# Kernel optimization log

Hardware: AMD Instinct MI355X
Metric: run time of the kernel (lower is better)

The kernel has to match this reference:

```python
import jax, jax.numpy as jnp
import numpy as np

D = 512
H = 8
DH = D // H  # 64


def setup_inputs() -> dict:
    key = jax.random.key(0)
    ks = jax.random.split(key, 7)
    batch, la, lb = 8, 256, 256
    A = jax.random.normal(ks[0], (batch, la, D), dtype=jnp.float32)
    B = jax.random.normal(ks[1], (batch, lb, D), dtype=jnp.float32)
    s = 1.0 / np.sqrt(D)
    W1 = jax.random.uniform(ks[2], (D, D), minval=-s, maxval=s, dtype=jnp.float32)
    b1 = jax.random.uniform(ks[3], (D,), minval=-s, maxval=s, dtype=jnp.float32)
    W2 = jax.random.uniform(ks[4], (D, D), minval=-s, maxval=s, dtype=jnp.float32)
    b2 = jax.random.uniform(ks[5], (D,), minval=-s, maxval=s, dtype=jnp.float32)
    q = jax.random.normal(ks[6], (DH,), dtype=jnp.float32) * 0.1
    return {"A": A, "B": B, "W1": W1, "b1": b1, "W2": W2, "b2": b2, "q": q}


def reference(A, B, W1, b1, W2, b2, q):
    bs, la, _ = A.shape
    lb = B.shape[1]
    # Linear + ReLU, then raw row-major reshape to (batch, heads, len, dh)
    # (matches torch .view semantics: NOT a head-transpose split)
    A_ = jax.nn.relu(A @ W1.T + b1).reshape(bs, H, la, DH)
    B_ = jax.nn.relu(B @ W2.T + b2).reshape(bs, H, lb, DH)
    # bilinear score: tanh of elementwise pairwise product, dotted with q
    # att_maps: [bs, H, la, lb]
    att_maps = jnp.einsum(
        "bhijc,c->bhij",
        jnp.tanh(A_[:, :, :, None, :] * B_[:, :, None, :, :]),
        q,
    )
    temp_b2a = jax.nn.softmax(jnp.mean(att_maps, axis=3), axis=2)  # [bs,H,la]
    temp_a2b = jax.nn.softmax(jnp.mean(att_maps, axis=2), axis=2)  # [bs,H,lb]
    A_heads = A.reshape(bs, H, la, DH)
    B_heads = B.reshape(bs, H, lb, DH)
    A_p = jnp.sum(A_heads * temp_b2a[..., None], axis=2).reshape(bs, -1)  # [bs, d]
    B_p = jnp.sum(B_heads * temp_a2b[..., None], axis=2).reshape(bs, -1)  # [bs, d]
    return (
        jnp.concatenate((A_p, B_p), axis=1),
        jnp.mean(temp_b2a, axis=1),
        jnp.mean(temp_a2b, axis=1),
    )
```

## Files before the change

kernel.cpp:

```cpp
#include <hip/hip_runtime.h>
#include <hip/hip_bf16.h>

#define LOG2E 1.4426950408889634f
#define SC2   2.8853900817779268f

typedef __attribute__((ext_vector_type(8))) short short8b;
typedef __attribute__((ext_vector_type(4))) float f32x4;

__device__ __forceinline__ float fast_exp2(float x) {
#if __has_builtin(__builtin_amdgcn_exp2f)
  return __builtin_amdgcn_exp2f(x);
#else
  return exp2f(x);
#endif
}
__device__ __forceinline__ float fast_rcp(float x) {
#if __has_builtin(__builtin_amdgcn_rcpf)
  return __builtin_amdgcn_rcpf(x);
#else
  return 1.0f / x;
#endif
}
__device__ __forceinline__ short f2bf(float f) {
  __hip_bfloat16 h = __float2bfloat16(f);
  return *reinterpret_cast<short*>(&h);
}

__global__ __launch_bounds__(256) void cvt_kernel(
    const float* __restrict__ A, const float* __restrict__ B,
    const float* __restrict__ W1, const float* __restrict__ W2,
    short* __restrict__ Abf, short* __restrict__ Bbf,
    short* __restrict__ W1bf, short* __restrict__ W2bf) {
  int gid = blockIdx.x * 256 + threadIdx.x;
  const float* src; short* dst; int off;
  if (gid < 131072)      { src = A;  dst = Abf;  off = gid << 3; }
  else if (gid < 262144) { src = B;  dst = Bbf;  off = (gid - 131072) << 3; }
  else if (gid < 294912) { src = W1; dst = W1bf; off = (gid - 262144) << 3; }
  else                   { src = W2; dst = W2bf; off = (gid - 294912) << 3; }
  float4 v0 = *reinterpret_cast<const float4*>(src + off);
  float4 v1 = *reinterpret_cast<const float4*>(src + off + 4);
  short8b s = {f2bf(v0.x), f2bf(v0.y), f2bf(v0.z), f2bf(v0.w),
               f2bf(v1.x), f2bf(v1.y), f2bf(v1.z), f2bf(v1.w)};
  *reinterpret_cast<short8b*>(dst + off) = s;
}

__global__ __launch_bounds__(256) void gemm_fused_kernel(
    const short* __restrict__ Xa, const short* __restrict__ Wa,
    const float* __restrict__ ba, float* __restrict__ Oa,
    const short* __restrict__ Xb, const short* __restrict__ Wb,
    const float* __restrict__ bb, const float* __restrict__ q,
    float2* __restrict__ Cb, unsigned* __restrict__ Cnt,
    float* __restrict__ Ksum) {
  const int isB = blockIdx.z;
  const short* X = isB ? Xb : Xa;
  const short* W = isB ? Wb : Wa;
  const float* bias = isB ? bb : ba;

  __shared__ __align__(16) float Btile[64][65];
  __shared__ float qls[64];

  int t = threadIdx.x;
  int m0 = blockIdx.x * 64, n0 = blockIdx.y * 64;
  int l = t & 63, w = t >> 6;
  int wm = (w >> 1) * 32, wn = (w & 1) * 32;
  int lr = l & 15, ko = (l >> 4) * 8;

  if (isB && t < 64) qls[t] = q[t];

  f32x4 acc[2][2];
#pragma unroll
  for (int m = 0; m < 2; ++m)
#pragma unroll
    for (int n = 0; n < 2; ++n) acc[m][n] = f32x4{0.f, 0.f, 0.f, 0.f};

  const short* pA = X + (m0 + wm + lr) * 512 + ko;
  const short* pW = W + (n0 + wn + lr) * 512 + ko;

#pragma unroll
  for (int k0 = 0; k0 < 512; k0 += 32) {
    short8b a0 = *reinterpret_cast<const short8b*>(pA + k0);
    short8b a1 = *reinterpret_cast<const short8b*>(pA + 8192 + k0);
    short8b b0 = *reinterpret_cast<const short8b*>(pW + k0);
    short8b b1 = *reinterpret_cast<const short8b*>(pW + 8192 + k0);
    acc[0][0] = __builtin_amdgcn_mfma_f32_16x16x32_bf16(a0, b0, acc[0][0], 0, 0, 0);
    acc[0][1] = __builtin_amdgcn_mfma_f32_16x16x32_bf16(a0, b1, acc[0][1], 0, 0, 0);
    acc[1][0] = __builtin_amdgcn_mfma_f32_16x16x32_bf16(a1, b0, acc[1][0], 0, 0, 0);
    acc[1][1] = __builtin_amdgcn_mfma_f32_16x16x32_bf16(a1, b1, acc[1][1], 0, 0, 0);
  }

  if (!isB) {
#pragma unroll
    for (int n = 0; n < 2; ++n) {
      int col = n0 + wn + n * 16 + lr;
      float bv = bias[col];
#pragma unroll
      for (int m = 0; m < 2; ++m) {
        int rbase = m0 + wm + m * 16 + (l >> 4) * 4;
#pragma unroll
        for (int r = 0; r < 4; ++r) {
          float v = acc[m][n][r] + bv;
          Oa[(rbase + r) * 512 + col] = v > 0.f ? v : 0.f;
        }
      }
    }
    return;
  }

#pragma unroll
  for (int n = 0; n < 2; ++n) {
    int col = wn + n * 16 + lr;
    float bv = bias[n0 + col];
#pragma unroll
    for (int m = 0; m < 2; ++m) {
      int rbase = wm + m * 16 + (l >> 4) * 4;
#pragma unroll
      for (int r = 0; r < 4; ++r) {
        float v = acc[m][n][r] + bv;
        Btile[rbase + r][col] = v > 0.f ? v : 0.f;
      }
    }
  }
  __syncthreads();

  int jl = t >> 2, p = t & 2 ? (t & 3) : (t & 3);
  p = t & 3;
  int row = m0 + jl;
  int bh = (row >> 8) * 8 + ((row >> 5) & 7);
  int j = ((row & 31) << 3) + (n0 >> 6);
  int c0 = p * 16;

  int nz = 0;
  float K = 0.f;
#pragma unroll
  for (int cc = 0; cc < 16; ++cc) {
    float v = Btile[jl][c0 + cc];
    if (v > 0.f) { ++nz; K += qls[c0 + cc]; }
  }
  int incl = nz;
#pragma unroll
  for (int d = 1; d < 4; d <<= 1) {
    int u = __shfl_up(incl, d, 4);
    if (p >= d) incl += u;
  }
  int off = incl - nz;
  int total = __shfl(incl, 3, 4);

  float2* dst = Cb + (bh * 256 + j) * 64;
  int k = off;
#pragma unroll
  for (int cc = 0; cc < 16; ++cc) {
    int c = c0 + cc;
    float v = Btile[jl][c];
    if (v > 0.f) {
      unsigned qb = (__float_as_uint(-2.f * qls[c]) & ~63u) | (unsigned)c;
      dst[k] = make_float2(v * SC2, __uint_as_float(qb));
      ++k;
    }
  }
  K += __shfl_xor(K, 1, 4);
  K += __shfl_xor(K, 2, 4);
  if (p == 3) {
    int cnt = total;
    while (cnt & 3) { dst[cnt] = make_float2(0.f, 0.f); ++cnt; }
    Cnt[bh * 256 + j] = (unsigned)cnt;
    Ksum[bh * 256 + j] = K;
  }
}

__global__ __launch_bounds__(512, 8) void attmap_kernel(
    const float* __restrict__ Ar, const float2* __restrict__ Cb,
    const unsigned* __restrict__ Cnt,
    float* __restrict__ rowpart, float* __restrict__ colsum) {
  int bh = blockIdx.x, jblk = blockIdx.y, isplit = blockIdx.z;
  int t = threadIdx.x;
  int il = t & 127;
  int g = __builtin_amdgcn_readfirstlane(t >> 7);
  __shared__ __align__(16) float Als[128 * 65];
  __shared__ float red[512];
  __shared__ float cpart[8][8];

  const float* Abase = Ar + bh * 16384 + isplit * 8192;
#pragma unroll
  for (int it = 0; it < 4; ++it) {
    int idx = it * 512 + t;
    int r = idx >> 4, c4 = (idx & 15) << 2;
    float4 v = *reinterpret_cast<const float4*>(&Abase[r * 64 + c4]);
    Als[r * 65 + c4 + 0] = v.x; Als[r * 65 + c4 + 1] = v.y;
    Als[r * 65 + c4 + 2] = v.z; Als[r * 65 + c4 + 3] = v.w;
  }
  __syncthreads();

  const float* Arow = &Als[il * 65];
  float acc[8];

#pragma unroll
  for (int jj = 0; jj < 8; ++jj) {
    int jl = g * 8 + jj;
    int n = (int)__builtin_amdgcn_readfirstlane(Cnt[bh * 256 + jblk * 32 + jl]);
    const float4* P4 = reinterpret_cast<const float4*>(Cb + (bh * 256 + jblk * 32 + jl) * 64);
    float s0 = 0.f, s1 = 0.f;
    if (n > 0) {
      const int nit = n >> 2;
      float4 u0 = P4[0], v0 = P4[1];
      int i1 = (1 < nit) ? 1 : (nit - 1);
      float4 u1 = P4[i1 * 2], v1 = P4[i1 * 2 + 1];
#pragma unroll 1
      for (int it = 0; it < nit; ++it) {
        int i2 = it + 2; i2 = (i2 < nit) ? i2 : (nit - 1);
        float4 u2 = P4[i2 * 2], v2 = P4[i2 * 2 + 1];
        float g0 = Arow[__float_as_uint(u0.y) & 63u];
        float g1 = Arow[__float_as_uint(u0.w) & 63u];
        float g2 = Arow[__float_as_uint(v0.y) & 63u];
        float g3 = Arow[__float_as_uint(v0.w) & 63u];
        float e0 = fast_exp2(g0 * u0.x);
        float e1 = fast_exp2(g1 * u0.z);
        float e2 = fast_exp2(g2 * v0.x);
        float e3 = fast_exp2(g3 * v0.z);
        float w0 = e0 + 1.f, w1 = e1 + 1.f, w2 = e2 + 1.f, w3 = e3 + 1.f;
        float n01 = fmaf(u0.w, w0, u0.y * w1);
        float n23 = fmaf(v0.w, w2, v0.y * w3);
        s0 = fmaf(n01, fast_rcp(w0 * w1), s0);
        s1 = fmaf(n23, fast_rcp(w2 * w3), s1);
        u0 = u1; v0 = v1; u1 = u2; v1 = v2;
      }
    }
    acc[jj] = s0 + s1;
  }

  float rs = 0.f;
#pragma unroll
  for (int jj = 0; jj < 8; ++jj) rs += acc[jj];
  red[t] = rs;

  int lane = t & 63, w = t >> 6;
#pragma unroll
  for (int jj = 0; jj < 8; ++jj) {
    float v = acc[jj];
#pragma unroll
    for (int off = 32; off >= 1; off >>= 1) v += __shfl_xor(v, off);
    if (lane == 0) cpart[w][jj] = v;
  }
  __syncthreads();
  if (t < 128) {
    rowpart[(bh * 8 + jblk) * 256 + isplit * 128 + t] =
        red[t] + red[t + 128] + red[t + 256] + red[t + 384];
  } else if (t < 160) {
    int jl = t - 128;
    int gg = jl >> 3, jj = jl & 7;
    colsum[(bh * 2 + isplit) * 256 + jblk * 32 + jl] =
        cpart[2 * gg][jj] + cpart[2 * gg + 1][jj];
  }
}

__global__ __launch_bounds__(512) void softmax_pool_kernel(
    const float* __restrict__ rowpart, const float* __restrict__ colsum,
    const float* __restrict__ Ksum,
    const float* __restrict__ A0, const float* __restrict__ B0,
    float* __restrict__ b2a, float* __restrict__ a2b,
    float* __restrict__ poolA, float* __restrict__ poolB) {
  int bh = blockIdx.x, chunk = blockIdx.y;
  int b = bh >> 3, h = bh & 7;
  int t = threadIdx.x;
  int tt = t & 255;
  int lane = t & 63, w = (t >> 6) & 3;
  __shared__ float redA[4], redB[4], redC[4], redD[4];
  __shared__ float tA[256], tB[256];
  __shared__ float pp[8][64];

  float r = 0.f;
#pragma unroll
  for (int jb = 0; jb < 8; ++jb) r += rowpart[(bh * 8 + jb) * 256 + tt];
  r *= (1.f / 256.f);
  float cs = Ksum[bh * 256 + tt] +
             (colsum[(bh * 2 + 0) * 256 + tt] + colsum[(bh * 2 + 1) * 256 + tt]) * (1.f / 256.f);

  float mr = r, mc = cs;
#pragma unroll
  for (int off = 32; off >= 1; off >>= 1) {
    mr = fmaxf(mr, __shfl_xor(mr, off));
    mc = fmaxf(mc, __shfl_xor(mc, off));
  }
  if (lane == 0) { redA[w] = mr; redB[w] = mc; }
  __syncthreads();
  mr = fmaxf(fmaxf(redA[0], redA[1]), fmaxf(redA[2], redA[3]));
  mc = fmaxf(fmaxf(redB[0], redB[1]), fmaxf(redB[2], redB[3]));

  float er = fast_exp2((r - mr) * LOG2E);
  float ec = fast_exp2((cs - mc) * LOG2E);
  float sr = er, sc = ec;
#pragma unroll
  for (int off = 32; off >= 1; off >>= 1) {
    sr += __shfl_xor(sr, off);
    sc += __shfl_xor(sc, off);
  }
  if (lane == 0) { redC[w] = sr; redD[w] = sc; }
  __syncthreads();
  sr = redC[0] + redC[1] + redC[2] + redC[3];
  sc = redD[0] + redD[1] + redD[2] + redD[3];

  float vb2a = er * fast_rcp(sr);
  float va2b = ec * fast_rcp(sc);
  tA[tt] = vb2a; tB[tt] = va2b;
  if (chunk == 0) {
    b2a[bh * 256 + tt] = vb2a;
    a2b[bh * 256 + tt] = va2b;
  }
  __syncthreads();

  int c = t & 63, isub = t >> 6;
  const float* Ab = A0 + b * 131072 + h * 16384;
  const float* Bb = B0 + b * 131072 + h * 16384;
  float pa = 0.f, pb = 0.f;
#pragma unroll
  for (int ii = 0; ii < 8; ++ii) {
    int i = chunk * 64 + isub * 8 + ii;
    pa = fmaf(Ab[i * 64 + c], tA[i], pa);
    pb = fmaf(Bb[i * 64 + c], tB[i], pb);
  }
  pp[isub][c] = pa;
  __syncthreads();
  if (t < 64) {
    float s = 0.f;
#pragma unroll
    for (int k = 0; k < 8; ++k) s += pp[k][t];
    poolA[(bh * 4 + chunk) * 64 + t] = s;
  }
  __syncthreads();
  pp[isub][c] = pb;
  __syncthreads();
  if (t < 64) {
    float s = 0.f;
#pragma unroll
    for (int k = 0; k < 8; ++k) s += pp[k][t];
    poolB[(bh * 4 + chunk) * 64 + t] = s;
  }
}

__global__ __launch_bounds__(256) void final_kernel(
    const float* __restrict__ poolA, const float* __restrict__ poolB,
    const float* __restrict__ b2a, const float* __restrict__ a2b,
    float* __restrict__ out) {
  int b = blockIdx.x, t = threadIdx.x;
  float s1 = 0.f, s2 = 0.f;
#pragma unroll
  for (int h = 0; h < 8; ++h) {
    s1 += b2a[(b * 8 + h) * 256 + t];
    s2 += a2b[(b * 8 + h) * 256 + t];
  }
  out[8192 + b * 256 + t] = s1 * 0.125f;
  out[10240 + b * 256 + t] = s2 * 0.125f;

#pragma unroll
  for (int hh = 0; hh < 2; ++hh) {
    int idx = hh * 256 + t;
    int h = idx >> 6, c = idx & 63;
    int base = ((b * 8 + h) * 4) * 64 + c;
    float sA = poolA[base] + poolA[base + 64] + poolA[base + 128] + poolA[base + 192];
    float sB = poolB[base] + poolB[base + 64] + poolB[base + 128] + poolB[base + 192];
    out[b * 1024 + h * 64 + c] = sA;
    out[b * 1024 + 512 + h * 64 + c] = sB;
  }
}

extern "C" void kernel_launch(void* const* d_in, const int* in_sizes, int n_in,
                              void* d_out, int out_size, void* d_ws, size_t ws_size,
                              hipStream_t stream) {
  const float* A  = (const float*)d_in[0];
  const float* B  = (const float*)d_in[1];
  const float* W1 = (const float*)d_in[2];
  const float* b1 = (const float*)d_in[3];
  const float* W2 = (const float*)d_in[4];
  const float* b2 = (const float*)d_in[5];
  const float* q  = (const float*)d_in[6];
  float* out = (float*)d_out;
  float* ws = (float*)d_ws;

  float*    Ar      = ws;
  short*    Abf     = (short*)(ws + 1048576);
  short*    Bbf     = (short*)(ws + 1572864);
  short*    W1bf    = (short*)(ws + 2097152);
  short*    W2bf    = (short*)(ws + 2228224);
  float2*   Cb      = (float2*)(ws + 2359296);
  unsigned* Cnt     = (unsigned*)(ws + 4456448);
  float*    Ksum    = ws + 4472832;
  float*    rowpart = ws + 4489216;
  float*    colsum  = ws + 4620288;
  float*    b2a     = ws + 4653056;
  float*    a2b     = ws + 4669440;
  float*    poolA   = ws + 4685824;
  float*    poolB   = ws + 4702208;

  cvt_kernel<<<1280, 256, 0, stream>>>(A, B, W1, W2, Abf, Bbf, W1bf, W2bf);
  gemm_fused_kernel<<<dim3(32, 8, 2), 256, 0, stream>>>(
      Abf, W1bf, b1, Ar, Bbf, W2bf, b2, q, Cb, Cnt, Ksum);
  attmap_kernel<<<dim3(64, 8, 2), 512, 0, stream>>>(Ar, Cb, Cnt, rowpart, colsum);
  softmax_pool_kernel<<<dim3(64, 4), 512, 0, stream>>>(
      rowpart, colsum, Ksum, A, B, b2a, a2b, poolA, poolB);
  final_kernel<<<8, 256, 0, stream>>>(poolA, poolB, b2a, a2b, out);
}
```

Before: 74.33 us.

## Stage GEMM tiles through LDS and enlarge block tile to 128x64

The fused linear GEMM now loads each 32-wide K slice of X and W into shared memory cooperatively, then feeds MFMA fragments from LDS instead of loading them directly from global memory per wave. The block tile grows from 64 to 128 rows, so each wave computes a 64x32 sub-tile, and the grid is halved. The compaction epilogue is remapped to two threads per row. This raises operand reuse and cuts redundant global loads, but adds two barriers per K step with no double buffering, uses more LDS, and launches fewer blocks (256 in total).

Result: faster. 70.18 us (-5.6%).

```diff
diff --git a/kernel.cpp b/kernel.cpp
--- a/kernel.cpp
+++ b/kernel.cpp
@@ -56,36 +56,53 @@
   const short* W = isB ? Wb : Wa;
   const float* bias = isB ? bb : ba;
 
-  __shared__ __align__(16) float Btile[64][65];
+  __shared__ __align__(16) short As[128 * 40];
+  __shared__ __align__(16) short Ws[64 * 40];
+  __shared__ __align__(16) float Btile[128][65];
   __shared__ float qls[64];
 
   int t = threadIdx.x;
-  int m0 = blockIdx.x * 64, n0 = blockIdx.y * 64;
+  int m0 = blockIdx.x * 128, n0 = blockIdx.y * 64;
   int l = t & 63, w = t >> 6;
-  int wm = (w >> 1) * 32, wn = (w & 1) * 32;
+  int wm = (w >> 1) * 64, wn = (w & 1) * 32;
   int lr = l & 15, ko = (l >> 4) * 8;
 
   if (isB && t < 64) qls[t] = q[t];
 
-  f32x4 acc[2][2];
-#pragma unroll
-  for (int m = 0; m < 2; ++m)
+  f32x4 acc[4][2];
+#pragma unroll
+  for (int m = 0; m < 4; ++m)
 #pragma unroll
     for (int n = 0; n < 2; ++n) acc[m][n] = f32x4{0.f, 0.f, 0.f, 0.f};
 
-  const short* pA = X + (m0 + wm + lr) * 512 + ko;
-  const short* pW = W + (n0 + wn + lr) * 512 + ko;
-
-#pragma unroll
   for (int k0 = 0; k0 < 512; k0 += 32) {
-    short8b a0 = *reinterpret_cast<const short8b*>(pA + k0);
-    short8b a1 = *reinterpret_cast<const short8b*>(pA + 8192 + k0);
-    short8b b0 = *reinterpret_cast<const short8b*>(pW + k0);
-    short8b b1 = *reinterpret_cast<const short8b*>(pW + 8192 + k0);
-    acc[0][0] = __builtin_amdgcn_mfma_f32_16x16x32_bf16(a0, b0, acc[0][0], 0, 0, 0);
-    acc[0][1] = __builtin_amdgcn_mfma_f32_16x16x32_bf16(a0, b1, acc[0][1], 0, 0, 0);
-    acc[1][0] = __builtin_amdgcn_mfma_f32_16x16x32_bf16(a1, b0, acc[1][0], 0, 0, 0);
-    acc[1][1] = __builtin_amdgcn_mfma_f32_16x16x32_bf16(a1, b1, acc[1][1], 0, 0, 0);
+#pragma unroll
+    for (int s = 0; s < 2; ++s) {
+      int slot = t + s * 256;
+      int row = slot >> 2, qd = (slot & 3) << 3;
+      *reinterpret_cast<short8b*>(&As[row * 40 + qd]) =
+          *reinterpret_cast<const short8b*>(&X[(m0 + row) * 512 + k0 + qd]);
+    }
+    {
+      int row = t >> 2, qd = (t & 3) << 3;
+      *reinterpret_cast<short8b*>(&Ws[row * 40 + qd]) =
+          *reinterpret_cast<const short8b*>(&W[(n0 + row) * 512 + k0 + qd]);
+    }
+    __syncthreads();
+
+    short8b afr[4], bfr[2];
+#pragma unroll
+    for (int m = 0; m < 4; ++m)
+      afr[m] = *reinterpret_cast<const short8b*>(&As[(wm + m * 16 + lr) * 40 + ko]);
+#pragma unroll
+    for (int n = 0; n < 2; ++n)
+      bfr[n] = *reinterpret_cast<const short8b*>(&Ws[(wn + n * 16 + lr) * 40 + ko]);
+#pragma unroll
+    for (int m = 0; m < 4; ++m)
+#pragma unroll
+      for (int n = 0; n < 2; ++n)
+        acc[m][n] = __builtin_amdgcn_mfma_f32_16x16x32_bf16(afr[m], bfr[n], acc[m][n], 0, 0, 0);
+    __syncthreads();
   }
 
   if (!isB) {
@@ -94,7 +111,7 @@
       int col = n0 + wn + n * 16 + lr;
       float bv = bias[col];
 #pragma unroll
-      for (int m = 0; m < 2; ++m) {
+      for (int m = 0; m < 4; ++m) {
         int rbase = m0 + wm + m * 16 + (l >> 4) * 4;
 #pragma unroll
         for (int r = 0; r < 4; ++r) {
@@ -111,7 +128,7 @@
     int col = wn + n * 16 + lr;
     float bv = bias[n0 + col];
 #pragma unroll
-    for (int m = 0; m < 2; ++m) {
+    for (int m = 0; m < 4; ++m) {
       int rbase = wm + m * 16 + (l >> 4) * 4;
 #pragma unroll
       for (int r = 0; r < 4; ++r) {
@@ -122,33 +139,31 @@
   }
   __syncthreads();
 
-  int jl = t >> 2, p = t & 2 ? (t & 3) : (t & 3);
-  p = t & 3;
+  int jl = t >> 1, p = t & 1;
   int row = m0 + jl;
   int bh = (row >> 8) * 8 + ((row >> 5) & 7);
   int j = ((row & 31) << 3) + (n0 >> 6);
-  int c0 = p * 16;
+  int c0 = p * 32;
 
   int nz = 0;
   float K = 0.f;
 #pragma unroll
-  for (int cc = 0; cc < 16; ++cc) {
+  for (int cc = 0; cc < 32; ++cc) {
     float v = Btile[jl][c0 + cc];
     if (v > 0.f) { ++nz; K += qls[c0 + cc]; }
   }
   int incl = nz;
-#pragma unroll
-  for (int d = 1; d < 4; d <<= 1) {
-    int u = __shfl_up(incl, d, 4);
-    if (p >= d) incl += u;
+  {
+    int u = __shfl_up(incl, 1, 2);
+    if (p >= 1) incl += u;
   }
   int off = incl - nz;
-  int total = __shfl(incl, 3, 4);
+  int total = __shfl(incl, 1, 2);
 
   float2* dst = Cb + (bh * 256 + j) * 64;
   int k = off;
-#pragma unroll
-  for (int cc = 0; cc < 16; ++cc) {
+#pragma unroll 4
+  for (int cc = 0; cc < 32; ++cc) {
     int c = c0 + cc;
     float v = Btile[jl][c];
     if (v > 0.f) {
@@ -157,9 +172,8 @@
       ++k;
     }
   }
-  K += __shfl_xor(K, 1, 4);
-  K += __shfl_xor(K, 2, 4);
-  if (p == 3) {
+  K += __shfl_xor(K, 1, 2);
+  if (p == 1) {
     int cnt = total;
     while (cnt & 3) { dst[cnt] = make_float2(0.f, 0.f); ++cnt; }
     Cnt[bh * 256 + j] = (unsigned)cnt;
@@ -391,7 +405,7 @@
   float*    poolB   = ws + 4702208;
 
   cvt_kernel<<<1280, 256, 0, stream>>>(A, B, W1, W2, Abf, Bbf, W1bf, W2bf);
-  gemm_fused_kernel<<<dim3(32, 8, 2), 256, 0, stream>>>(
+  gemm_fused_kernel<<<dim3(16, 8, 2), 256, 0, stream>>>(
       Abf, W1bf, b1, Ar, Bbf, W2bf, b2, q, Cb, Cnt, Ksum);
   attmap_kernel<<<dim3(64, 8, 2), 512, 0, stream>>>(Ar, Cb, Cnt, rowpart, colsum);
   softmax_pool_kernel<<<dim3(64, 4), 512, 0, stream>>>(
```
